# Performance work log

Measured on AMD Instinct MI355X. Metric: run time of the kernel, lower is better.

Reference implementation:

```python
import jax, jax.numpy as jnp
import numpy as np

HEADS = 16
DIM_HEAD = 64

def setup_inputs() -> dict:
    key = jax.random.key(0)
    ks = jax.random.split(key, 5)
    B, S, D = 2, 2048, 1024
    return {
        "hidden_states": jax.random.normal(ks[0], (B, S, D), dtype=jnp.float32),
        "Wq": jax.random.normal(ks[1], (D, D), dtype=jnp.float32) * (D ** -0.5),
        "Wkv": jax.random.normal(ks[2], (D, D), dtype=jnp.float32) * (D ** -0.5),
        "Wout": jax.random.normal(ks[3], (D, D), dtype=jnp.float32) * (D ** -0.5),
        "bout": jnp.zeros((D,), dtype=jnp.float32),
    }

def reference(hidden_states, Wq, Wkv, Wout, bout):
    B, S, D = hidden_states.shape
    H, Dh = HEADS, DIM_HEAD
    # projections (torch Linear: x @ W.T; here weights are stored as [in, out])
    q = hidden_states @ Wq            # [B, S, D]
    kv = hidden_states @ Wkv          # key == value share the to_kv projection
    q = q.reshape(B, S, H, Dh).transpose(0, 2, 1, 3)   # [B, H, S, Dh]
    k = kv.reshape(B, S, H, Dh).transpose(0, 2, 1, 3)
    v = k
    scale = 1.0 / np.sqrt(Dh).astype(np.float32)
    # ReLU attention: no softmax
    attn = jax.nn.relu(jnp.einsum("bhsd,bhtd->bhst", q, k) * scale)  # [B,H,S,S]
    out = jnp.einsum("bhst,bhtd->bhsd", attn, v)                     # [B,H,S,Dh]
    out = out.transpose(0, 2, 1, 3).reshape(B, S, H * Dh)
    return out @ Wout + bout
```

## Files before the change

### kernel.cpp

```cpp
#include <hip/hip_runtime.h>
#include <hip/hip_bf16.h>

#define HEADS  16
#define DIMH   64
#define NBATCH 2
#define SEQ    2048
#define DMODEL 1024
#define MROWS  (NBATCH * SEQ)

typedef __attribute__((ext_vector_type(8)))  short bf16x8;
typedef __attribute__((ext_vector_type(4)))  float f32x4;
typedef __attribute__((ext_vector_type(16))) float f32x16;
typedef __attribute__((ext_vector_type(4)))  float float4v;
typedef __attribute__((ext_vector_type(4)))  short short4v;
typedef __attribute__((ext_vector_type(8)))  short short8v;

__device__ inline void glds16(const void* g, void* l) {
    __builtin_amdgcn_global_load_lds(
        (const __attribute__((address_space(1))) unsigned int*)g,
        (__attribute__((address_space(3))) unsigned int*)l, 16, 0, 0);
}

#define WAIT_VMCNT(N) asm volatile("s_waitcnt vmcnt(" #N ")" ::: "memory")
#define BARRIER() do { __builtin_amdgcn_s_barrier(); asm volatile("" ::: "memory"); } while (0)

__global__ void prep_kernel(const float* __restrict__ hs,
                            const float* __restrict__ Wq,
                            const float* __restrict__ Wkv,
                            const float* __restrict__ Wout,
                            __hip_bfloat16* __restrict__ hsb,
                            __hip_bfloat16* __restrict__ WqT,
                            __hip_bfloat16* __restrict__ WkvT,
                            __hip_bfloat16* __restrict__ WoT) {
    __shared__ float tile[64][65];
    const int tid = threadIdx.x;
    const int bid = blockIdx.x;
    if (bid < 768) {
        const int w = bid >> 8;
        const int tnum = bid & 255;
        const int bx = tnum & 15;
        const int by = tnum >> 4;
        const float* __restrict__ W = (w == 0) ? Wq : (w == 1) ? Wkv : Wout;
        __hip_bfloat16* __restrict__ WT = (w == 0) ? WqT : (w == 1) ? WkvT : WoT;
        const int ty = tid >> 6, tx = tid & 63;
#pragma unroll
        for (int r = 0; r < 16; ++r)
            tile[ty * 16 + r][tx] = W[(size_t)(by * 64 + ty * 16 + r) * DMODEL + bx * 64 + tx];
        __syncthreads();
#pragma unroll
        for (int r = 0; r < 16; ++r)
            WT[(size_t)(bx * 64 + ty * 16 + r) * DMODEL + by * 64 + tx] =
                __float2bfloat16(tile[tx][ty * 16 + r]);
    } else {
        const int cb = bid - 768;
#pragma unroll
        for (int jj = 0; jj < 4; ++jj) {
            int i = cb * 1024 + jj * 256 + tid;
            float4v v = reinterpret_cast<const float4v*>(hs)[i];
            union { short4v s; __hip_bfloat16 h[4]; } u;
#pragma unroll
            for (int j = 0; j < 4; ++j) u.h[j] = __float2bfloat16(v[j]);
            reinterpret_cast<short4v*>(hsb)[i] = u.s;
        }
    }
}

__global__ void combine_kernel(const __hip_bfloat16* __restrict__ p0,
                               const __hip_bfloat16* __restrict__ p1,
                               __hip_bfloat16* __restrict__ out, int n8) {
    int i = blockIdx.x * blockDim.x + threadIdx.x;
    if (i >= n8) return;
    union { short8v s; __hip_bfloat16 h[8]; } a, b, u;
    a.s = reinterpret_cast<const short8v*>(p0)[i];
    b.s = reinterpret_cast<const short8v*>(p1)[i];
#pragma unroll
    for (int j = 0; j < 8; ++j)
        u.h[j] = __float2bfloat16(__bfloat162float(a.h[j]) + __bfloat162float(b.h[j]));
    reinterpret_cast<short8v*>(out)[i] = u.s;
}

__launch_bounds__(512, 4)
__global__ void proj_kernel(const __hip_bfloat16* __restrict__ hsb,
                            const __hip_bfloat16* __restrict__ WqT,
                            const __hip_bfloat16* __restrict__ WkvT,
                            __hip_bfloat16* __restrict__ qb,
                            __hip_bfloat16* __restrict__ kb,
                            __hip_bfloat16* __restrict__ vtb) {
    __shared__ __align__(16) char SLDS[49152];
    char (*Alds)[8192] = (char (*)[8192])SLDS;
    char (*Blds)[8192] = (char (*)[8192])(SLDS + 24576);
    char* CT = SLDS;

    const int tid  = threadIdx.x;
    const int wave = tid >> 6;
    const int lane = tid & 63;
    const int lr = lane & 15;
    const int lk = lane >> 4;
    const int wm = wave >> 1, wn = wave & 1;

    int bid = blockIdx.x;
    bid = (bid & 7) * 64 + (bid >> 3);
    const int xt = bid & 15;
    const int mt = bid >> 4;
    const bool is_q = xt < 8;
    const int mbase = mt * 128;
    const int nbase = (xt & 7) * 128;
    const __hip_bfloat16* __restrict__ WT = is_q ? WqT : WkvT;

    const char* __restrict__ Ab = (const char*)(hsb + (size_t)mbase * DMODEL);
    const char* __restrict__ Bb = (const char*)(WT + (size_t)nbase * DMODEL);

    auto stage = [&](int buf, int k0) {
        const size_t colb = (size_t)k0 * 2 + lk * 16;
        const size_t rowoff = (size_t)(wave * 16 + lr) * (DMODEL * 2);
        glds16(Ab + rowoff + colb, &Alds[buf][wave * 1024]);
        glds16(Bb + rowoff + colb, &Blds[buf][wave * 1024]);
    };

    stage(0, 0);
    stage(1, 32);

    f32x4 acc[2][4] = {};
    int c0 = 0;
    for (int t = 0; t < DMODEL / 32; ++t) {
        if (t < DMODEL / 32 - 1) WAIT_VMCNT(2); else WAIT_VMCNT(0);
        BARRIER();
        if (t + 2 < DMODEL / 32) {
            int sb = c0 + 2; if (sb >= 3) sb -= 3;
            stage(sb, (t + 2) * 32);
        }
        bf16x8 af[2], bfr[4];
#pragma unroll
        for (int i = 0; i < 2; ++i)
            af[i] = *reinterpret_cast<const bf16x8*>(&Alds[c0][(wm * 2 + i) * 1024 + lane * 16]);
#pragma unroll
        for (int j = 0; j < 4; ++j)
            bfr[j] = *reinterpret_cast<const bf16x8*>(&Blds[c0][(wn * 4 + j) * 1024 + lane * 16]);
#pragma unroll
        for (int i = 0; i < 2; ++i)
#pragma unroll
            for (int j = 0; j < 4; ++j)
                acc[i][j] = __builtin_amdgcn_mfma_f32_16x16x32_bf16(af[i], bfr[j], acc[i][j], 0, 0, 0);
        c0 = (c0 + 1 == 3) ? 0 : c0 + 1;
    }

    const float qscale = is_q ? 0.125f : 1.0f;
    const int b_ = mbase >> 11;
    const int s0 = mbase & (SEQ - 1);
    const int h0 = nbase >> 6;
    BARRIER();

#pragma unroll
    for (int i = 0; i < 2; ++i)
#pragma unroll
        for (int j = 0; j < 4; ++j)
#pragma unroll
            for (int r = 0; r < 4; ++r) {
                int m = wm * 32 + i * 16 + lk * 4 + r;
                int n = wn * 64 + j * 16 + lr;
                *reinterpret_cast<__hip_bfloat16*>(
                    &CT[m * 256 + ((n * 2) ^ (((m >> 2) & 7) << 4))]) =
                    __float2bfloat16(acc[i][j][r] * qscale);
            }
    BARRIER();

    __hip_bfloat16* __restrict__ dst0 = is_q ? qb : kb;
#pragma unroll
    for (int p = 0; p < 4; ++p) {
        int g = p * 64 + (tid >> 3);
        int m = g >> 1, hseg = g & 1, o = tid & 7;
        int key = ((m >> 2) & 7) << 4;
        bf16x8 val = *reinterpret_cast<const bf16x8*>(
            &CT[m * 256 + ((hseg * 128 + o * 16) ^ key)]);
        *reinterpret_cast<bf16x8*>(
            &dst0[(((size_t)b_ * HEADS + h0 + hseg) * SEQ + s0 + m) * DIMH + o * 8]) = val;
    }

    if (!is_q) {
        BARRIER();
#pragma unroll
        for (int i = 0; i < 2; ++i)
#pragma unroll
            for (int j = 0; j < 4; ++j)
#pragma unroll
                for (int r = 0; r < 4; ++r) {
                    int m = wm * 32 + i * 16 + lk * 4 + r;
                    int n = wn * 64 + j * 16 + lr;
                    *reinterpret_cast<__hip_bfloat16*>(
                        &CT[n * 256 + ((m * 2) ^ ((n & 7) << 4))]) =
                        __float2bfloat16(acc[i][j][r]);
                }
        BARRIER();
#pragma unroll
        for (int p = 0; p < 4; ++p) {
            int g = p * 64 + (tid >> 3);
            int n = g >> 1, half = g & 1, o = tid & 7;
            int key2 = (n & 7) << 4;
            int D = half * 64 + o * 8;
            int mm = D >> 4, H = o & 1;
            union { unsigned long long d[2]; bf16x8 v; } val;
            val.d[0] = *reinterpret_cast<const unsigned long long*>(
                &CT[n * 256 + ((mm * 32 + H * 8) ^ key2)]);
            val.d[1] = *reinterpret_cast<const unsigned long long*>(
                &CT[n * 256 + ((mm * 32 + 16 + H * 8) ^ key2)]);
            int h = h0 + (n >> 6);
            int dh = n & 63;
            *reinterpret_cast<bf16x8*>(
                &vtb[(((size_t)b_ * HEADS + h) * DIMH + dh) * SEQ + s0 + D]) = val.v;
        }
    }
}

__launch_bounds__(512, 4)
__global__ void outproj_kernel(const __hip_bfloat16* __restrict__ ao,
                               const __hip_bfloat16* __restrict__ WoT,
                               const float* __restrict__ bout,
                               float* __restrict__ out) {
    __shared__ __align__(16) char Alds[3][4096];
    __shared__ __align__(16) char Blds[3][8192];
    const int tid  = threadIdx.x;
    const int wave = tid >> 6;
    const int lane = tid & 63;
    const int lr = lane & 15;
    const int lk = lane >> 4;
    const int wm = wave >> 2, wn = wave & 3;

    int bid = blockIdx.x;
    bid = (bid & 7) * 64 + (bid >> 3);
    const int xt = bid & 7;
    const int mt = bid >> 3;
    const int mbase = mt * 64;
    const int nbase = xt * 128;

    const char* __restrict__ Ab = (const char*)(ao + (size_t)mbase * DMODEL);
    const char* __restrict__ Bb = (const char*)(WoT + (size_t)nbase * DMODEL);

    auto stage = [&](int buf, int k0) {
        const size_t colb = (size_t)k0 * 2 + lk * 16;
        if (wave < 4)
            glds16(Ab + (size_t)(wave * 16 + lr) * (DMODEL * 2) + colb,
                   &Alds[buf][wave * 1024]);
        glds16(Bb + (size_t)(wave * 16 + lr) * (DMODEL * 2) + colb,
               &Blds[buf][wave * 1024]);
    };

    stage(0, 0);
    stage(1, 32);

    f32x4 acc[2][2] = {};
    int c0 = 0;
    for (int t = 0; t < DMODEL / 32; ++t) {
        if (t < DMODEL / 32 - 1) {
            if (wave < 4) WAIT_VMCNT(2); else WAIT_VMCNT(1);
        } else WAIT_VMCNT(0);
        BARRIER();
        if (t + 2 < DMODEL / 32) {
            int sb = c0 + 2; if (sb >= 3) sb -= 3;
            stage(sb, (t + 2) * 32);
        }
        bf16x8 af[2], bfr[2];
#pragma unroll
        for (int i = 0; i < 2; ++i)
            af[i] = *reinterpret_cast<const bf16x8*>(&Alds[c0][(wm * 2 + i) * 1024 + lane * 16]);
#pragma unroll
        for (int j = 0; j < 2; ++j)
            bfr[j] = *reinterpret_cast<const bf16x8*>(&Blds[c0][(wn * 2 + j) * 1024 + lane * 16]);
#pragma unroll
        for (int i = 0; i < 2; ++i)
#pragma unroll
            for (int j = 0; j < 2; ++j)
                acc[i][j] = __builtin_amdgcn_mfma_f32_16x16x32_bf16(af[i], bfr[j], acc[i][j], 0, 0, 0);
        c0 = (c0 + 1 == 3) ? 0 : c0 + 1;
    }

#pragma unroll
    for (int j = 0; j < 2; ++j) {
        const int n = nbase + wn * 32 + j * 16 + lr;
        const float bias = bout[n];
#pragma unroll
        for (int i = 0; i < 2; ++i) {
#pragma unroll
            for (int r = 0; r < 4; ++r) {
                int m = mbase + wm * 32 + i * 16 + lk * 4 + r;
                out[(size_t)m * DMODEL + n] = acc[i][j][r] + bias;
            }
        }
    }
}

__launch_bounds__(512, 2)
__global__ void attn_kernel(const __hip_bfloat16* __restrict__ qb,
                            const __hip_bfloat16* __restrict__ kb,
                            const __hip_bfloat16* __restrict__ vtb,
                            __hip_bfloat16* __restrict__ po) {
    __shared__ __align__(16) char Klds[3][16384];
    __shared__ __align__(16) char Vlds[3][16384];
    const int lane = threadIdx.x & 63;
    const int wave = threadIdx.x >> 6;
    const int l32  = lane & 31;
    const int hi   = lane >> 5;

    int bid = blockIdx.x;
    bid = (bid & 7) * 32 + (bid >> 3);
    const int ts   = bid & 1;
    const int qblk = (bid >> 1) & 3;
    const int bh   = bid >> 3;
    const int b_ = bh >> 4, h = bh & 15;
    const int qbase = qblk * 512 + wave * 64;
    const int tbeg = ts * (SEQ / 2);

    const __hip_bfloat16* __restrict__ Q = qb + (size_t)bh * SEQ * DIMH;
    const char* __restrict__ Kg = (const char*)(kb  + (size_t)bh * SEQ * DIMH);
    const char* __restrict__ Vg = (const char*)(vtb + (size_t)bh * DIMH * SEQ);

    bf16x8 qf[2][4];
#pragma unroll
    for (int g = 0; g < 2; ++g)
#pragma unroll
        for (int ks = 0; ks < 4; ++ks)
            qf[g][ks] = *reinterpret_cast<const bf16x8*>(
                &Q[(size_t)(qbase + g * 32 + l32) * DIMH + ks * 16 + hi * 8]);

    auto stage = [&](int buf, int t0) {
        const int krow = (wave >> 2) * 32 + l32;
        const int kcol = (wave & 3) * 32 + hi * 16;
        glds16(Kg + (size_t)(t0 + krow) * 128 + kcol,       &Klds[buf][wave * 1024]);
        glds16(Kg + (size_t)(t0 + 64 + krow) * 128 + kcol,  &Klds[buf][(8 + wave) * 1024]);
        const size_t vrow = (size_t)((wave & 1) * 32 + l32) * (SEQ * 2);
        const int vcol = (wave >> 1) * 32 + hi * 16;
        glds16(Vg + vrow + (size_t)t0 * 2 + vcol,           &Vlds[buf][wave * 1024]);
        glds16(Vg + vrow + (size_t)(t0 + 64) * 2 + vcol,    &Vlds[buf][(8 + wave) * 1024]);
    };

    f32x16 acco[2][2] = {};

    auto compute = [&](const char* Kc, const char* Vc, int u) {
        const int ro = u * 8192;
        f32x16 sp[2][2] = {};
        __builtin_amdgcn_s_setprio(1);
#pragma unroll
        for (int ks = 0; ks < 4; ++ks) {
            bf16x8 k0f = *reinterpret_cast<const bf16x8*>(Kc + ro + ks * 1024 + lane * 16);
            bf16x8 k1f = *reinterpret_cast<const bf16x8*>(Kc + ro + (4 + ks) * 1024 + lane * 16);
            sp[0][0] = __builtin_amdgcn_mfma_f32_32x32x16_bf16(k0f, qf[0][ks], sp[0][0], 0, 0, 0);
            sp[0][1] = __builtin_amdgcn_mfma_f32_32x32x16_bf16(k1f, qf[0][ks], sp[0][1], 0, 0, 0);
            sp[1][0] = __builtin_amdgcn_mfma_f32_32x32x16_bf16(k0f, qf[1][ks], sp[1][0], 0, 0, 0);
            sp[1][1] = __builtin_amdgcn_mfma_f32_32x32x16_bf16(k1f, qf[1][ks], sp[1][1], 0, 0, 0);
        }
#pragma unroll
        for (int kt = 0; kt < 4; ++kt) {
            bf16x8 v0 = *reinterpret_cast<const bf16x8*>(Vc + ro + (kt * 2 + 0) * 1024 + lane * 16);
            bf16x8 v1 = *reinterpret_cast<const bf16x8*>(Vc + ro + (kt * 2 + 1) * 1024 + lane * 16);
            const int rb = (kt & 1) * 8;
#pragma unroll
            for (int g = 0; g < 2; ++g) {
                union { __hip_bfloat16 hh[8]; bf16x8 v; } pa;
#pragma unroll
                for (int j = 0; j < 8; ++j) {
                    float x = (kt < 2) ? sp[g][0][rb + j] : sp[g][1][rb + j];
                    pa.hh[j] = __float2bfloat16(fmaxf(x, 0.f));
                }
                acco[g][0] = __builtin_amdgcn_mfma_f32_32x32x16_bf16(pa.v, v0, acco[g][0], 0, 0, 0);
                acco[g][1] = __builtin_amdgcn_mfma_f32_32x32x16_bf16(pa.v, v1, acco[g][1], 0, 0, 0);
            }
        }
        __builtin_amdgcn_s_setprio(0);
    };

    const int NT = SEQ / 2 / 128;
    stage(0, tbeg);
    stage(1, tbeg + 128);

    for (int t = 0; t < NT; ++t) {
        if (t < NT - 1) WAIT_VMCNT(4); else WAIT_VMCNT(0);
        BARRIER();
        if (t + 2 < NT) {
            int sb = t + 2; sb -= (sb / 3) * 3;
            stage(sb, tbeg + (t + 2) * 128);
        }
        const int c0 = t % 3;
        compute(Klds[c0], Vlds[c0], 0);
        compute(Klds[c0], Vlds[c0], 1);
    }

    __hip_bfloat16* __restrict__ PO = po + (size_t)ts * MROWS * DMODEL;
#pragma unroll
    for (int g = 0; g < 2; ++g)
#pragma unroll
        for (int nt = 0; nt < 2; ++nt)
#pragma unroll
            for (int r = 0; r < 16; ++r) {
                int q = qbase + g * 32 + (r & 3) + 8 * (r >> 2) + 4 * hi;
                PO[(size_t)(b_ * SEQ + q) * DMODEL + h * 64 + nt * 32 + l32] =
                    __float2bfloat16(acco[g][nt][r]);
            }
}

extern "C" void kernel_launch(void* const* d_in, const int* in_sizes, int n_in,
                              void* d_out, int out_size, void* d_ws, size_t ws_size,
                              hipStream_t stream) {
    const float* hs   = (const float*)d_in[0];
    const float* Wq   = (const float*)d_in[1];
    const float* Wkv  = (const float*)d_in[2];
    const float* Wout = (const float*)d_in[3];
    const float* bout = (const float*)d_in[4];
    float* out = (float*)d_out;

    char* ws = (char*)d_ws;
    size_t off = 0;
    auto alloc = [&](size_t bytes) { char* p = ws + off; off += bytes; return p; };
    __hip_bfloat16* hsb  = (__hip_bfloat16*)alloc((size_t)MROWS * DMODEL * 2);
    __hip_bfloat16* WqT  = (__hip_bfloat16*)alloc((size_t)DMODEL * DMODEL * 2);
    __hip_bfloat16* WkvT = (__hip_bfloat16*)alloc((size_t)DMODEL * DMODEL * 2);
    __hip_bfloat16* WoT  = (__hip_bfloat16*)alloc((size_t)DMODEL * DMODEL * 2);
    __hip_bfloat16* qb   = (__hip_bfloat16*)alloc((size_t)MROWS * DMODEL * 2);
    __hip_bfloat16* kb   = (__hip_bfloat16*)alloc((size_t)MROWS * DMODEL * 2);
    __hip_bfloat16* vtb  = (__hip_bfloat16*)alloc((size_t)MROWS * DMODEL * 2);
    __hip_bfloat16* po   = (__hip_bfloat16*)alloc((size_t)2 * MROWS * DMODEL * 2);
    __hip_bfloat16* ao   = hsb;

    prep_kernel<<<1792, 256, 0, stream>>>(hs, Wq, Wkv, Wout, hsb, WqT, WkvT, WoT);

    proj_kernel<<<512, 512, 0, stream>>>(hsb, WqT, WkvT, qb, kb, vtb);

    attn_kernel<<<256, 512, 0, stream>>>(qb, kb, vtb, po);

    combine_kernel<<<(MROWS * DMODEL / 8 + 255) / 256, 256, 0, stream>>>(
        po, po + (size_t)MROWS * DMODEL, ao, MROWS * DMODEL / 8);

    outproj_kernel<<<512, 512, 0, stream>>>(ao, WoT, bout, out);
}
```

Measured before the change: 112.4 us.

## Switch projection GEMMs to double-buffered 64-wide K steps

Both the QKV projection and output projection kernels now stage 64 K-elements per iteration into two LDS buffers instead of 32 K-elements into a triple-buffered ring. This halves the number of loop iterations and barrier/wait points and issues more loads per stage. In exchange, prefetch depth drops to one stage ahead, a second barrier is added per iteration, and the projection kernel's LDS use grows to 64 KB, which may reduce occupancy.

```diff
diff --git a/kernel.cpp b/kernel.cpp
--- a/kernel.cpp
+++ b/kernel.cpp
@@ -86,9 +86,9 @@
                             __hip_bfloat16* __restrict__ qb,
                             __hip_bfloat16* __restrict__ kb,
                             __hip_bfloat16* __restrict__ vtb) {
-    __shared__ __align__(16) char SLDS[49152];
-    char (*Alds)[8192] = (char (*)[8192])SLDS;
-    char (*Blds)[8192] = (char (*)[8192])(SLDS + 24576);
+    __shared__ __align__(16) char SLDS[65536];
+    char (*Alds)[16384] = (char (*)[16384])SLDS;
+    char (*Blds)[16384] = (char (*)[16384])(SLDS + 32768);
     char* CT = SLDS;
 
     const int tid  = threadIdx.x;
@@ -111,44 +111,48 @@
     const char* __restrict__ Bb = (const char*)(WT + (size_t)nbase * DMODEL);
 
     auto stage = [&](int buf, int k0) {
-        const size_t colb = (size_t)k0 * 2 + lk * 16;
         const size_t rowoff = (size_t)(wave * 16 + lr) * (DMODEL * 2);
-        glds16(Ab + rowoff + colb, &Alds[buf][wave * 1024]);
-        glds16(Bb + rowoff + colb, &Blds[buf][wave * 1024]);
+        const size_t c0b = (size_t)k0 * 2 + lk * 16;
+        const size_t c1b = (size_t)(k0 + 32) * 2 + lk * 16;
+        glds16(Ab + rowoff + c0b, &Alds[buf][wave * 1024]);
+        glds16(Ab + rowoff + c1b, &Alds[buf][8192 + wave * 1024]);
+        glds16(Bb + rowoff + c0b, &Blds[buf][wave * 1024]);
+        glds16(Bb + rowoff + c1b, &Blds[buf][8192 + wave * 1024]);
     };
 
     stage(0, 0);
-    stage(1, 32);
 
     f32x4 acc[2][4] = {};
-    int c0 = 0;
-    for (int t = 0; t < DMODEL / 32; ++t) {
-        if (t < DMODEL / 32 - 1) WAIT_VMCNT(2); else WAIT_VMCNT(0);
-        BARRIER();
-        if (t + 2 < DMODEL / 32) {
-            int sb = c0 + 2; if (sb >= 3) sb -= 3;
-            stage(sb, (t + 2) * 32);
-        }
-        bf16x8 af[2], bfr[4];
-#pragma unroll
-        for (int i = 0; i < 2; ++i)
-            af[i] = *reinterpret_cast<const bf16x8*>(&Alds[c0][(wm * 2 + i) * 1024 + lane * 16]);
-#pragma unroll
-        for (int j = 0; j < 4; ++j)
-            bfr[j] = *reinterpret_cast<const bf16x8*>(&Blds[c0][(wn * 4 + j) * 1024 + lane * 16]);
-#pragma unroll
-        for (int i = 0; i < 2; ++i)
+    const int NT = DMODEL / 64;
+    for (int t = 0; t < NT; ++t) {
+        if (t + 1 < NT) stage((t + 1) & 1, (t + 1) * 64);
+        if (t + 1 < NT) WAIT_VMCNT(4); else WAIT_VMCNT(0);
+        BARRIER();
+        const int c0 = t & 1;
+#pragma unroll
+        for (int kc = 0; kc < 2; ++kc) {
+            bf16x8 af[2], bfr[4];
+#pragma unroll
+            for (int i = 0; i < 2; ++i)
+                af[i] = *reinterpret_cast<const bf16x8*>(
+                    &Alds[c0][kc * 8192 + (wm * 2 + i) * 1024 + lane * 16]);
 #pragma unroll
             for (int j = 0; j < 4; ++j)
-                acc[i][j] = __builtin_amdgcn_mfma_f32_16x16x32_bf16(af[i], bfr[j], acc[i][j], 0, 0, 0);
-        c0 = (c0 + 1 == 3) ? 0 : c0 + 1;
+                bfr[j] = *reinterpret_cast<const bf16x8*>(
+                    &Blds[c0][kc * 8192 + (wn * 4 + j) * 1024 + lane * 16]);
+#pragma unroll
+            for (int i = 0; i < 2; ++i)
+#pragma unroll
+                for (int j = 0; j < 4; ++j)
+                    acc[i][j] = __builtin_amdgcn_mfma_f32_16x16x32_bf16(af[i], bfr[j], acc[i][j], 0, 0, 0);
+        }
+        BARRIER();
     }
 
     const float qscale = is_q ? 0.125f : 1.0f;
     const int b_ = mbase >> 11;
     const int s0 = mbase & (SEQ - 1);
     const int h0 = nbase >> 6;
-    BARRIER();
 
 #pragma unroll
     for (int i = 0; i < 2; ++i)
@@ -216,8 +220,8 @@
                                const __hip_bfloat16* __restrict__ WoT,
                                const float* __restrict__ bout,
                                float* __restrict__ out) {
-    __shared__ __align__(16) char Alds[3][4096];
-    __shared__ __align__(16) char Blds[3][8192];
+    __shared__ __align__(16) char Alds[2][8192];
+    __shared__ __align__(16) char Blds[2][16384];
     const int tid  = threadIdx.x;
     const int wave = tid >> 6;
     const int lane = tid & 63;
@@ -236,41 +240,41 @@
     const char* __restrict__ Bb = (const char*)(WoT + (size_t)nbase * DMODEL);
 
     auto stage = [&](int buf, int k0) {
-        const size_t colb = (size_t)k0 * 2 + lk * 16;
-        if (wave < 4)
-            glds16(Ab + (size_t)(wave * 16 + lr) * (DMODEL * 2) + colb,
-                   &Alds[buf][wave * 1024]);
-        glds16(Bb + (size_t)(wave * 16 + lr) * (DMODEL * 2) + colb,
-               &Blds[buf][wave * 1024]);
+        const size_t acol = (size_t)(k0 + (wave >> 2) * 32) * 2 + lk * 16;
+        glds16(Ab + (size_t)((wave & 3) * 16 + lr) * (DMODEL * 2) + acol,
+               &Alds[buf][(wave >> 2) * 4096 + (wave & 3) * 1024]);
+        const size_t rowoff = (size_t)(wave * 16 + lr) * (DMODEL * 2);
+        glds16(Bb + rowoff + (size_t)k0 * 2 + lk * 16,        &Blds[buf][wave * 1024]);
+        glds16(Bb + rowoff + (size_t)(k0 + 32) * 2 + lk * 16, &Blds[buf][8192 + wave * 1024]);
     };
 
     stage(0, 0);
-    stage(1, 32);
 
     f32x4 acc[2][2] = {};
-    int c0 = 0;
-    for (int t = 0; t < DMODEL / 32; ++t) {
-        if (t < DMODEL / 32 - 1) {
-            if (wave < 4) WAIT_VMCNT(2); else WAIT_VMCNT(1);
-        } else WAIT_VMCNT(0);
-        BARRIER();
-        if (t + 2 < DMODEL / 32) {
-            int sb = c0 + 2; if (sb >= 3) sb -= 3;
-            stage(sb, (t + 2) * 32);
-        }
-        bf16x8 af[2], bfr[2];
-#pragma unroll
-        for (int i = 0; i < 2; ++i)
-            af[i] = *reinterpret_cast<const bf16x8*>(&Alds[c0][(wm * 2 + i) * 1024 + lane * 16]);
-#pragma unroll
-        for (int j = 0; j < 2; ++j)
-            bfr[j] = *reinterpret_cast<const bf16x8*>(&Blds[c0][(wn * 2 + j) * 1024 + lane * 16]);
-#pragma unroll
-        for (int i = 0; i < 2; ++i)
+    const int NT = DMODEL / 64;
+    for (int t = 0; t < NT; ++t) {
+        if (t + 1 < NT) stage((t + 1) & 1, (t + 1) * 64);
+        if (t + 1 < NT) WAIT_VMCNT(3); else WAIT_VMCNT(0);
+        BARRIER();
+        const int c0 = t & 1;
+#pragma unroll
+        for (int kc = 0; kc < 2; ++kc) {
+            bf16x8 af[2], bfr[2];
+#pragma unroll
+            for (int i = 0; i < 2; ++i)
+                af[i] = *reinterpret_cast<const bf16x8*>(
+                    &Alds[c0][kc * 4096 + (wm * 2 + i) * 1024 + lane * 16]);
 #pragma unroll
             for (int j = 0; j < 2; ++j)
-                acc[i][j] = __builtin_amdgcn_mfma_f32_16x16x32_bf16(af[i], bfr[j], acc[i][j], 0, 0, 0);
-        c0 = (c0 + 1 == 3) ? 0 : c0 + 1;
+                bfr[j] = *reinterpret_cast<const bf16x8*>(
+                    &Blds[c0][kc * 8192 + (wn * 2 + j) * 1024 + lane * 16]);
+#pragma unroll
+            for (int i = 0; i < 2; ++i)
+#pragma unroll
+                for (int j = 0; j < 2; ++j)
+                    acc[i][j] = __builtin_amdgcn_mfma_f32_16x16x32_bf16(af[i], bfr[j], acc[i][j], 0, 0, 0);
+        }
+        BARRIER();
     }
 
 #pragma unroll
```

After: 110.5 us, median of 2. No clear change (-1.7%).
